# Performance work log

Measured on AMD Instinct MI355X. Metric: run time of the kernel, lower is better.

The kernel has to match this reference:

```python
import jax, jax.numpy as jnp
import numpy as np

DIM = 384
HEADS = 12
WIN = (2, 7, 7)
MLP_RATIO = 4.0
EPS = 1e-5


def _rel_index(Wt, Wh, Ww):
    t, h, w = np.meshgrid(np.arange(Wt), np.arange(Wh), np.arange(Ww), indexing='ij')
    coords = np.stack([t, h, w]).reshape(3, -1).T  # (N,3)
    rel = coords[:, None] - coords[None]  # (N,N,3)
    rel[..., 0] += Wt - 1
    rel[..., 1] += Wh - 1
    rel[..., 2] += Ww - 1
    rel[..., 0] *= (2 * Wh - 1) * (2 * Ww - 1)
    rel[..., 1] *= (2 * Ww - 1)
    return rel.sum(-1)  # (N,N) int


def setup_inputs() -> dict:
    key = jax.random.key(0)
    ks = jax.random.split(key, 16)
    d = DIM
    hdim = int(d * MLP_RATIO)
    Wt, Wh, Ww = WIN
    table_size = (2 * Wt - 1) * (2 * Wh - 1) * (2 * Ww - 1)
    s = lambda fan: 1.0 / np.sqrt(fan)
    return {
        'x': jax.random.normal(ks[0], (2, 8, 56, 56, d), jnp.float32),
        'norm1_g': jnp.ones((d,), jnp.float32),
        'norm1_b': jnp.zeros((d,), jnp.float32),
        'qkv_w': jax.random.normal(ks[1], (d, 3 * d), jnp.float32) * s(d),
        'qkv_b': jnp.zeros((3 * d,), jnp.float32),
        'proj_w': jax.random.normal(ks[2], (d, d), jnp.float32) * s(d),
        'proj_b': jnp.zeros((d,), jnp.float32),
        'bias_table': jax.random.normal(ks[3], (table_size, HEADS), jnp.float32) * 0.02,
        'norm2_g': jnp.ones((d,), jnp.float32),
        'norm2_b': jnp.zeros((d,), jnp.float32),
        'fc1_w': jax.random.normal(ks[4], (d, hdim), jnp.float32) * s(d),
        'fc1_b': jnp.zeros((hdim,), jnp.float32),
        'fc2_w': jax.random.normal(ks[5], (hdim, d), jnp.float32) * s(hdim),
        'fc2_b': jnp.zeros((d,), jnp.float32),
        'rel_index': jnp.asarray(_rel_index(*WIN), jnp.int32),
    }


def _ln(x, g, b):
    mu = x.mean(-1, keepdims=True)
    var = ((x - mu) ** 2).mean(-1, keepdims=True)
    return (x - mu) * jax.lax.rsqrt(var + EPS) * g + b


def _window_partition(x, win):
    B, T, H, W, C = x.shape
    Wt, Wh, Ww = win
    x = x.reshape(B, T // Wt, Wt, H // Wh, Wh, W // Ww, Ww, C)
    x = x.transpose(0, 1, 3, 5, 2, 4, 6, 7)
    return x.reshape(-1, Wt * Wh * Ww, C)


def _window_reverse(win_x, win, B, T, H, W):
    Wt, Wh, Ww = win
    C = win_x.shape[-1]
    x = win_x.reshape(B, T // Wt, H // Wh, W // Ww, Wt, Wh, Ww, C)
    x = x.transpose(0, 1, 4, 2, 5, 3, 6, 7)
    return x.reshape(B, T, H, W, C)


def reference(x, norm1_g, norm1_b, qkv_w, qkv_b, proj_w, proj_b, bias_table,
              norm2_g, norm2_b, fc1_w, fc1_b, fc2_w, fc2_b, rel_index):
    B, T, H, W, C = x.shape
    Wt, Wh, Ww = WIN
    N = Wt * Wh * Ww
    shift = (Wt // 2, Wh // 2, Ww // 2)
    head_dim = C // HEADS
    scale = head_dim ** -0.5

    shortcut = x
    h = _ln(x, norm1_g, norm1_b)
    h = jnp.roll(h, shift=(-shift[0], -shift[1], -shift[2]), axis=(1, 2, 3))
    # dims chosen divisible by window -> no padding branch
    wins = _window_partition(h, WIN)  # (BnW, N, C)
    BnW = wins.shape[0]

    qkv = wins @ qkv_w + qkv_b  # (BnW, N, 3C)
    qkv = qkv.reshape(BnW, N, 3, HEADS, head_dim).transpose(2, 0, 3, 1, 4)
    q, k, v = qkv[0] * scale, qkv[1], qkv[2]  # (BnW, H, N, d)

    bias = bias_table[rel_index.reshape(-1)].reshape(N, N, HEADS).transpose(2, 0, 1)
    attn = jnp.einsum('bhnd,bhmd->bhnm', q, k) + bias[None]
    attn = jax.nn.softmax(attn, axis=-1)
    out = jnp.einsum('bhnm,bhmd->bhnd', attn, v)
    out = out.transpose(0, 2, 1, 3).reshape(BnW, N, C)
    out = out @ proj_w + proj_b

    h = _window_reverse(out.reshape(-1, Wt, Wh, Ww, C), WIN, B, T, H, W)
    h = jnp.roll(h, shift=shift, axis=(1, 2, 3))
    x = shortcut + h

    h2 = _ln(x, norm2_g, norm2_b)
    h2 = jax.nn.gelu(h2 @ fc1_w + fc1_b, approximate=False) @ fc2_w + fc2_b
    return x + h2
```

## Files before the change

### kernel.cpp

```cpp
#include <hip/hip_runtime.h>
#include <cstdint>
#include <cstddef>


typedef __bf16 bf16x8 __attribute__((ext_vector_type(8)));
typedef __bf16 bf16x4 __attribute__((ext_vector_type(4)));
typedef float f32x4 __attribute__((ext_vector_type(4)));

#define DIM 384
#define QKV_DIM 1152
#define HID 1536
#define NHEADS 12
#define NTOK 50176
#define NWIN 512

__device__ __forceinline__ void gload16(const void* g, void* s) {
  __builtin_amdgcn_global_load_lds(
      (const __attribute__((address_space(1))) void*)g,
      (__attribute__((address_space(3))) void*)s, 16, 0, 0);
}

__global__ __launch_bounds__(256) void build_tokmap_k(int* __restrict__ map) {
  int t = blockIdx.x * 256 + threadIdx.x;
  if (t >= NTOK) return;
  int win = t / 98, n = t - win * 98;
  int b = win >> 8, tw = (win >> 6) & 3, hw = (win >> 3) & 7, ww = win & 7;
  int dt = n / 49; int rem = n - dt * 49; int dh = rem / 7, dw = rem - dh * 7;
  int t0 = (tw * 2 + dt + 1) & 7;
  int h0 = hw * 7 + dh + 3; if (h0 >= 56) h0 -= 56;
  int w0 = ww * 7 + dw + 3; if (w0 >= 56) w0 -= 56;
  map[t] = ((b * 8 + t0) * 56 + h0) * 56 + w0;
}

__global__ __launch_bounds__(256) void expand_biasp_k(const float* __restrict__ table,
                                                      const int* __restrict__ rel,
                                                      float* __restrict__ out) {
  int e = blockIdx.x * 256 + threadIdx.x;
  if (e >= NHEADS * 49 * 256) return;
  int r = e & 3, l = (e >> 2) & 63;
  int rest = e >> 8;
  int ni = rest % 7, mi = (rest / 7) % 7, h = rest / 49;
  int i = mi * 16 + (l >> 4) * 4 + r;
  int j = ni * 16 + (l & 15);
  float v;
  if (j >= 98) v = -1e30f;
  else if (i >= 98) v = 0.f;
  else v = table[rel[i * 98 + j] * NHEADS + h];
  out[e] = v;
}

__global__ __launch_bounds__(256) void pack_w64_k(const float* __restrict__ W,
                                                  __bf16* __restrict__ WP,
                                                  int K, int N, int nk,
                                                  int scaleCols, float scale) {
  int idx = blockIdx.x * 256 + threadIdx.x;
  if (idx >= (K * N) >> 3) return;
  int l = idx & 63, f = (idx >> 6) & 7;
  int rest = idx >> 9, kt = rest % nk, cn = rest / nk;
  int n = f >> 1, kk = f & 1;
  int col = cn * 64 + n * 16 + (l & 15);
  int k0 = kt * 64 + (kk * 4 + (l >> 4)) * 8;
  float sc = (col < scaleCols) ? scale : 1.0f;
  bf16x8 v;
  #pragma unroll
  for (int j = 0; j < 8; ++j)
    v[j] = (__bf16)(W[(size_t)(k0 + j) * N + col] * sc);
  *(bf16x8*)(WP + (size_t)idx * 8) = v;
}

__global__ __launch_bounds__(256) void scale_bias_k(const float* __restrict__ b,
                                                    float* __restrict__ out,
                                                    int n, int scaleCols, float scale) {
  int e = blockIdx.x * 256 + threadIdx.x;
  if (e >= n) return;
  out[e] = b[e] * (e < scaleCols ? scale : 1.0f);
}

__global__ __launch_bounds__(384) void vtrans_k(const __bf16* __restrict__ qkv,
                                                __bf16* __restrict__ vt) {
  __shared__ __align__(1024) char T[98304];
  int win = blockIdx.x, t = threadIdx.x;
  const __bf16* base = qkv + (size_t)win * 98 * QKV_DIM + 768 + t;
  #pragma unroll
  for (int c = 0; c < 16; ++c) {
    bf16x8 pk;
    #pragma unroll
    for (int e2 = 0; e2 < 8; ++e2) {
      int tok = c * 8 + e2;
      pk[e2] = (tok < 98) ? base[(size_t)tok * QKV_DIM] : (__bf16)0.f;
    }
    *(bf16x8*)(T + t * 256 + ((c ^ (t & 15)) << 4)) = pk;
  }
  __syncthreads();
  char* wb = (char*)(vt + (size_t)win * 49152);
  #pragma unroll
  for (int i = 0; i < 16; ++i) {
    int g = i * 6144 + t * 16;
    int row = g >> 8, p = (g >> 4) & 15;
    bf16x8 v = *(const bf16x8*)(T + row * 256 + (p << 4));
    int lc = p ^ (row & 15);
    *(bf16x8*)(wb + row * 256 + (lc << 4)) = v;
  }
}

template <typename T, bool MAP>
__global__ __launch_bounds__(256) void ln_pack_k(const T* __restrict__ x,
                                                 const float* __restrict__ g,
                                                 const float* __restrict__ bta,
                                                 __bf16* __restrict__ outp,
                                                 const int* __restrict__ map) {
  const int w = threadIdx.x >> 6, l = threadIdx.x & 63;
  const int tok = blockIdx.x * 32 + w * 8 + (l >> 3);
  const int src = MAP ? map[tok] : tok;
  const T* row = x + (size_t)src * DIM;
  const int o0 = l & 7;
  float v[6][8];
  float s = 0.f;
  #pragma unroll
  for (int j = 0; j < 6; ++j) {
    const int c = (o0 + 8 * j) * 8;
    if constexpr (sizeof(T) == 4) {
      f32x4 p0 = *(const f32x4*)(row + c);
      f32x4 p1 = *(const f32x4*)(row + c + 4);
      #pragma unroll
      for (int e = 0; e < 4; ++e) { v[j][e] = p0[e]; v[j][e + 4] = p1[e]; }
    } else {
      bf16x8 p = *(const bf16x8*)(row + c);
      #pragma unroll
      for (int e = 0; e < 8; ++e) v[j][e] = (float)p[e];
    }
    #pragma unroll
    for (int e = 0; e < 8; ++e) s += v[j][e];
  }
  s += __shfl_xor(s, 1, 64); s += __shfl_xor(s, 2, 64); s += __shfl_xor(s, 4, 64);
  const float mu = s * (1.f / DIM);
  float var = 0.f;
  #pragma unroll
  for (int j = 0; j < 6; ++j)
    #pragma unroll
    for (int e = 0; e < 8; ++e) { float d = v[j][e] - mu; var += d * d; }
  var += __shfl_xor(var, 1, 64); var += __shfl_xor(var, 2, 64); var += __shfl_xor(var, 4, 64);
  const float rs = rsqrtf(var * (1.f / DIM) + 1e-5f);
  const int mg = tok >> 6, m = (tok >> 4) & 3, lr = tok & 15;
  const int kk = o0 >> 2, lg = o0 & 3;
  __bf16* dst = outp + (size_t)mg * 24576 + (m * 2 + kk) * 512 + (lg * 16 + lr) * 8;
  #pragma unroll
  for (int j = 0; j < 6; ++j) {
    const int c = (o0 + 8 * j) * 8;
    f32x4 g0 = *(const f32x4*)(g + c), g1 = *(const f32x4*)(g + c + 4);
    f32x4 b0 = *(const f32x4*)(bta + c), b1 = *(const f32x4*)(bta + c + 4);
    bf16x8 ov;
    #pragma unroll
    for (int e = 0; e < 4; ++e) {
      ov[e] = (__bf16)((v[j][e] - mu) * rs * g0[e] + b0[e]);
      ov[e + 4] = (__bf16)((v[j][e + 4] - mu) * rs * g1[e] + b1[e]);
    }
    *(bf16x8*)(dst + (size_t)j * 4096) = ov;
  }
}

template <int EPI>
__global__ __launch_bounds__(256) void gemm_stream_k(const __bf16* __restrict__ AP,
                                                     const __bf16* __restrict__ WP,
                                                     const float* __restrict__ bias,
                                                     int N,
                                                     __bf16* __restrict__ outb) {
  __shared__ __align__(1024) char lds[32768];
  const int tid = threadIdx.x;
  const int l = tid & 63, w = tid >> 6;
  const int lr = l & 15, lg = l >> 4;
  const int ntile = N >> 6;
  const int nwg = gridDim.x, qd = nwg >> 3, rm = nwg & 7;
  const int xcd = blockIdx.x & 7;
  const int wgid = (xcd < rm ? xcd * (qd + 1) : rm * (qd + 1) + (xcd - rm) * qd)
                   + (blockIdx.x >> 3);
  const int bm = wgid / ntile, bn = wgid - bm * ntile;
  const int mg = bm * 4 + w;
  const int m0 = mg << 6, n0 = bn << 6;
  const __bf16* pA = AP + (size_t)mg * 24576 + l * 8;
  const __bf16* pB = WP + (size_t)bn * 24576 + l * 8;

  bf16x8 a[2][8], b[2][8];
  f32x4 acc[4][4] = {};
  #pragma unroll
  for (int f = 0; f < 8; ++f) {
    a[0][f] = *(const bf16x8*)(pA + f * 512);
    b[0][f] = *(const bf16x8*)(pB + f * 512);
  }
  #pragma unroll
  for (int kt = 0; kt < 6; ++kt) {
    const int cur = kt & 1, nxt = cur ^ 1;
    if (kt < 5) {
      const size_t ko = (size_t)(kt + 1) * 4096;
      #pragma unroll
      for (int f = 0; f < 8; ++f) {
        a[nxt][f] = *(const bf16x8*)(pA + ko + f * 512);
        b[nxt][f] = *(const bf16x8*)(pB + ko + f * 512);
      }
      asm volatile("s_waitcnt vmcnt(16)" ::: "memory");
    } else {
      asm volatile("s_waitcnt vmcnt(0)" ::: "memory");
    }
    __builtin_amdgcn_sched_barrier(0);
    __builtin_amdgcn_s_setprio(1);
    #pragma unroll
    for (int kk = 0; kk < 2; ++kk)
      #pragma unroll
      for (int m = 0; m < 4; ++m)
        #pragma unroll
        for (int n = 0; n < 4; ++n)
          acc[m][n] = __builtin_amdgcn_mfma_f32_16x16x32_bf16(
              b[cur][n * 2 + kk], a[cur][m * 2 + kk], acc[m][n], 0, 0, 0);
    __builtin_amdgcn_s_setprio(0);
  }

  char* abuf = lds + (w << 13);
  #pragma unroll
  for (int m = 0; m < 4; ++m) {
    const int row = (m << 4) + lr;
    #pragma unroll
    for (int n = 0; n < 4; ++n) {
      const int gcol = n0 + (n << 4) + (lg << 2);
      f32x4 a4 = acc[m][n] + *(const f32x4*)(bias + gcol);
      bf16x4 c;
      if (EPI == 2) {
        #pragma unroll
        for (int r = 0; r < 4; ++r) {
          float vv = a4[r];
          float y = vv * (1.0f + 0.044715f * vv * vv);
          c[r] = (__bf16)(vv / (1.0f + __expf(-1.5957691216057308f * y)));
        }
      } else {
        #pragma unroll
        for (int r = 0; r < 4; ++r) c[r] = (__bf16)a4[r];
      }
      const int ch = (n << 1) + (lg >> 1);
      *(bf16x4*)(abuf + (row << 7) + ((ch ^ (row & 7)) << 4) + ((lg & 1) << 3)) = c;
    }
  }
  asm volatile("s_waitcnt lgkmcnt(0)" ::: "memory");
  __builtin_amdgcn_sched_barrier(0);
  #pragma unroll
  for (int i = 0; i < 8; ++i) {
    const int row = (i << 3) + (l >> 3);
    const int p = (l & 7) ^ (row & 7);
    bf16x8 v = *(const bf16x8*)(abuf + (row << 7) + (p << 4));
    *(bf16x8*)(outb + (size_t)(m0 + row) * N + n0 + ((l & 7) << 3)) = v;
  }
}

template <int EPI>
__global__ __launch_bounds__(256) void gemm_k(const __bf16* __restrict__ A,
                                              const __bf16* __restrict__ WP,
                                              const float* __restrict__ bias,
                                              int M, int N, int K,
                                              __bf16* __restrict__ outb,
                                              float* __restrict__ outf,
                                              const float* __restrict__ residf,
                                              const __bf16* __restrict__ residb,
                                              const int* __restrict__ tokmap) {
  __shared__ __align__(1024) char lds[32768];
  const int tid = threadIdx.x;
  const int l = tid & 63, w = tid >> 6;
  const int lr = l & 15, lg = l >> 4;
  const int ntile = N >> 6;
  const int nwg = gridDim.x, qd = nwg >> 3, rm = nwg & 7;
  const int xcd = blockIdx.x & 7;
  const int wgid = (xcd < rm ? xcd * (qd + 1) : rm * (qd + 1) + (xcd - rm) * qd)
                   + (blockIdx.x >> 3);
  const int bm = wgid / ntile, bn = wgid - bm * ntile;
  const int m0 = (bm << 8) + (w << 6);
  const int n0 = bn << 6;
  const int nk = K >> 6;
  const int sch = (l & 7) ^ ((l >> 3) & 7);
  const __bf16* pa = A + (size_t)(m0 + (l >> 3)) * K + sch * 8;
  char* abuf = lds + (w << 13);
  const __bf16* pB = WP + (size_t)bn * nk * 4096 + l * 8;

#define STAGEA(kt)                                                   \
  { const size_t ko_ = (size_t)(kt) << 6;                            \
    _Pragma("unroll")                                                \
    for (int s_ = 0; s_ < 8; ++s_)                                   \
      gload16(pa + (size_t)(s_ * 8) * K + ko_, abuf + s_ * 1024); }
#define LOADB(kt)                                                    \
  { const __bf16* p_ = pB + (size_t)(kt) * 4096;                     \
    _Pragma("unroll")                                                \
    for (int f_ = 0; f_ < 8; ++f_)                                   \
      b[f_] = *(const bf16x8*)(p_ + f_ * 512); }
#define LDA()                                                        \
  { _Pragma("unroll")                                                \
    for (int kk_ = 0; kk_ < 2; ++kk_) {                              \
      const int ck_ = (kk_ << 2) + lg;                               \
      _Pragma("unroll")                                              \
      for (int m_ = 0; m_ < 4; ++m_) {                               \
        int r_ = (m_ << 4) + lr;                                     \
        a[m_][kk_] = *(const bf16x8*)(abuf + (r_ << 7) +             \
                                      ((ck_ ^ (r_ & 7)) << 4));      \
      } }                                                            \
    asm volatile("s_waitcnt lgkmcnt(0)" ::: "memory");               \
    __builtin_amdgcn_sched_barrier(0); }

  bf16x8 a[4][2], b[8];
  f32x4 acc[4][4] = {};
  STAGEA(0)
  asm volatile("s_waitcnt vmcnt(0)" ::: "memory");
  LDA()
  for (int kt = 0; kt < nk; ++kt) {
    LOADB(kt)
    const bool pf = (kt + 1 < nk);
    if (pf) STAGEA(kt + 1)
    __builtin_amdgcn_s_setprio(1);
    #pragma unroll
    for (int kk = 0; kk < 2; ++kk)
      #pragma unroll
      for (int m = 0; m < 4; ++m)
        #pragma unroll
        for (int n = 0; n < 4; ++n)
          acc[m][n] = __builtin_amdgcn_mfma_f32_16x16x32_bf16(b[n * 2 + kk], a[m][kk],
                                                              acc[m][n], 0, 0, 0);
    __builtin_amdgcn_s_setprio(0);
    if (pf) {
      asm volatile("s_waitcnt vmcnt(0)" ::: "memory");
      LDA()
    }
  }
#undef STAGEA
#undef LOADB
#undef LDA

  if (EPI == 3) {
    #pragma unroll
    for (int hh = 0; hh < 2; ++hh) {
      #pragma unroll
      for (int m = 0; m < 4; ++m) {
        const int row = (m << 4) + lr;
        #pragma unroll
        for (int n2 = 0; n2 < 2; ++n2) {
          const int n = (hh << 1) + n2;
          const int gcol = n0 + (n << 4) + (lg << 2);
          f32x4 a4 = acc[m][n] + *(const f32x4*)(bias + gcol);
          const int ch = (n2 << 2) + lg;
          *(f32x4*)(abuf + (row << 7) + ((ch ^ (row & 7)) << 4)) = a4;
        }
      }
      asm volatile("s_waitcnt lgkmcnt(0)" ::: "memory");
      __builtin_amdgcn_sched_barrier(0);
      #pragma unroll
      for (int i = 0; i < 8; ++i) {
        const int row = (i << 3) + (l >> 3);
        const int p = (l & 7) ^ (row & 7);
        f32x4 v = *(const f32x4*)(abuf + (row << 7) + (p << 4));
        const int grow = m0 + row;
        const int gcol = n0 + (hh << 5) + ((l & 7) << 2);
        bf16x4 sv = *(const bf16x4*)(residb + (size_t)grow * N + gcol);
        f32x4 o;
        #pragma unroll
        for (int r = 0; r < 4; ++r) o[r] = v[r] + (float)sv[r];
        *(f32x4*)(outf + (size_t)grow * N + gcol) = o;
      }
      if (hh == 0) {
        asm volatile("s_waitcnt lgkmcnt(0)" ::: "memory");
        __builtin_amdgcn_sched_barrier(0);
      }
    }
  } else {
    #pragma unroll
    for (int m = 0; m < 4; ++m) {
      const int row = (m << 4) + lr;
      #pragma unroll
      for (int n = 0; n < 4; ++n) {
        const int gcol = n0 + (n << 4) + (lg << 2);
        f32x4 a4 = acc[m][n] + *(const f32x4*)(bias + gcol);
        bf16x4 c;
        #pragma unroll
        for (int r = 0; r < 4; ++r) c[r] = (__bf16)a4[r];
        const int ch = (n << 1) + (lg >> 1);
        *(bf16x4*)(abuf + (row << 7) + ((ch ^ (row & 7)) << 4) + ((lg & 1) << 3)) = c;
      }
    }
    asm volatile("s_waitcnt lgkmcnt(0)" ::: "memory");
    __builtin_amdgcn_sched_barrier(0);
    #pragma unroll
    for (int i = 0; i < 8; ++i) {
      const int row = (i << 3) + (l >> 3);
      const int p = (l & 7) ^ (row & 7);
      bf16x8 v = *(const bf16x8*)(abuf + (row << 7) + (p << 4));
      const int gcol = n0 + ((l & 7) << 3);
      const int dst = tokmap[m0 + row];
      const float* rp = residf + (size_t)dst * N + gcol;
      f32x4 r0 = *(const f32x4*)rp, r1 = *(const f32x4*)(rp + 4);
      bf16x8 c2;
      #pragma unroll
      for (int j = 0; j < 4; ++j) {
        c2[j] = (__bf16)(r0[j] + (float)v[j]);
        c2[j + 4] = (__bf16)(r1[j] + (float)v[j + 4]);
      }
      *(bf16x8*)(outb + (size_t)dst * N + gcol) = c2;
    }
  }
}

__global__ __launch_bounds__(64) void attn_k(const __bf16* __restrict__ qkv,
                                             const __bf16* __restrict__ vt,
                                             const float* __restrict__ pb,
                                             __bf16* __restrict__ out) {
  __shared__ __align__(1024) char P[4096];
  const int l = threadIdx.x, lr = l & 15, lg = l >> 4;
  const int bid = blockIdx.x;
  const int xc = bid & 7, kk = bid >> 3;
  const int wh = (kk / 7) * 8 + xc, mi = kk % 7;
  const int win = wh / NHEADS, h = wh - win * NHEADS;
  const size_t wbase = (size_t)win * 98 * QKV_DIM;
  const __bf16* qb = qkv + wbase + h * 32;
  const __bf16* kb = qb + 384;
  const bf16x8 z8 = {};
  const f32x4 fz = {};

  bf16x8 kf[7];
  #pragma unroll
  for (int ni = 0; ni < 7; ++ni) {
    int tok = ni * 16 + lr;
    kf[ni] = (tok < 98) ? *(const bf16x8*)(kb + (size_t)tok * QKV_DIM + lg * 8) : z8;
  }
  int qt = mi * 16 + lr;
  bf16x8 qf = (qt < 98) ? *(const bf16x8*)(qb + (size_t)qt * QKV_DIM + lg * 8) : z8;
  const f32x4* pbp = (const f32x4*)pb + (size_t)((h * 7 + mi) * 7) * 64 + l;
  f32x4 bv[7];
  #pragma unroll
  for (int ni = 0; ni < 7; ++ni) bv[ni] = pbp[ni * 64];

  f32x4 s[7];
  #pragma unroll
  for (int ni = 0; ni < 7; ++ni)
    s[ni] = __builtin_amdgcn_mfma_f32_16x16x32_bf16(qf, kf[ni], fz, 0, 0, 0);

  if (l < 32) {
    int row = l >> 1, c = 14 + (l & 1);
    *(f32x4*)(P + row * 256 + ((c ^ (row & 7)) << 4)) = fz;
  }

  #pragma unroll
  for (int r = 0; r < 4; ++r) {
    float mx = -1e30f;
    #pragma unroll
    for (int ni = 0; ni < 7; ++ni) {
      float vv = s[ni][r] + bv[ni][r];
      s[ni][r] = vv;
      mx = fmaxf(mx, vv);
    }
    #pragma unroll
    for (int m2 = 1; m2 < 16; m2 <<= 1) mx = fmaxf(mx, __shfl_xor(mx, m2, 64));
    float sum = 0.f;
    #pragma unroll
    for (int ni = 0; ni < 7; ++ni) { float p = __expf(s[ni][r] - mx); s[ni][r] = p; sum += p; }
    #pragma unroll
    for (int m2 = 1; m2 < 16; m2 <<= 1) sum += __shfl_xor(sum, m2, 64);
    float inv = 1.0f / sum;
    int il = lg * 4 + r;
    #pragma unroll
    for (int ni = 0; ni < 7; ++ni) {
      int j = ni * 16 + lr;
      *(__bf16*)(P + il * 256 + (((j >> 3) ^ (il & 7)) << 4) + ((j & 7) << 1)) =
          (__bf16)(s[ni][r] * inv);
    }
  }
  __syncthreads();

  bf16x8 pa[4];
  #pragma unroll
  for (int ks = 0; ks < 4; ++ks) {
    int ck = ks * 4 + lg;
    pa[ks] = *(const bf16x8*)(P + lr * 256 + ((ck ^ (lr & 7)) << 4));
  }
  const __bf16* vrow = vt + ((size_t)wh * 32) * 128;
  f32x4 oo[2];
  #pragma unroll
  for (int nf = 0; nf < 2; ++nf) {
    int d = nf * 16 + lr;
    f32x4 o = fz;
    #pragma unroll
    for (int ks = 0; ks < 4; ++ks) {
      bf16x8 vb = *(const bf16x8*)(vrow + (size_t)d * 128 + ks * 32 + lg * 8);
      o = __builtin_amdgcn_mfma_f32_16x16x32_bf16(pa[ks], vb, o, 0, 0, 0);
    }
    oo[nf] = o;
  }
  #pragma unroll
  for (int nf = 0; nf < 2; ++nf)
    #pragma unroll
    for (int r = 0; r < 4; ++r)
      *(__bf16*)(P + (lg * 4 + r) * 64 + (((nf << 4) + lr) << 1)) = (__bf16)oo[nf][r];
  asm volatile("s_waitcnt lgkmcnt(0)" ::: "memory");
  __builtin_amdgcn_sched_barrier(0);
  {
    const int row = l >> 2;
    bf16x8 v = *(const bf16x8*)(P + row * 64 + ((l & 3) << 4));
    const int tok = mi * 16 + row;
    if (tok < 98)
      *(bf16x8*)(out + ((size_t)win * 98 + tok) * DIM + h * 32 + ((l & 3) << 3)) = v;
  }
}

extern "C" void kernel_launch(void* const* d_in, const int* in_sizes, int n_in,
                              void* d_out, int out_size, void* d_ws, size_t ws_size,
                              hipStream_t stream) {
  const float* x      = (const float*)d_in[0];
  const float* n1g    = (const float*)d_in[1];
  const float* n1b    = (const float*)d_in[2];
  const float* qkv_w  = (const float*)d_in[3];
  const float* qkv_b  = (const float*)d_in[4];
  const float* proj_w = (const float*)d_in[5];
  const float* proj_b = (const float*)d_in[6];
  const float* btab   = (const float*)d_in[7];
  const float* n2g    = (const float*)d_in[8];
  const float* n2b    = (const float*)d_in[9];
  const float* fc1_w  = (const float*)d_in[10];
  const float* fc1_b  = (const float*)d_in[11];
  const float* fc2_w  = (const float*)d_in[12];
  const float* fc2_b  = (const float*)d_in[13];
  const int*   relidx = (const int*)d_in[14];
  float* outp = (float*)d_out;
  (void)in_sizes; (void)n_in; (void)out_size; (void)ws_size;

  char* ws = (char*)d_ws;
  size_t off = 0;
  auto alloc = [&](size_t bytes) {
    char* p = ws + off;
    off = (off + bytes + 255) & ~(size_t)255;
    return p;
  };
  int*    tokmap  = (int*)alloc((size_t)NTOK * 4);
  float*  biasex  = (float*)alloc((size_t)NHEADS * 49 * 256 * 4);
  __bf16* wqkvP   = (__bf16*)alloc((size_t)QKV_DIM * DIM * 2);
  __bf16* wprojP  = (__bf16*)alloc((size_t)DIM * DIM * 2);
  __bf16* wfc1P   = (__bf16*)alloc((size_t)HID * DIM * 2);
  __bf16* wfc2P   = (__bf16*)alloc((size_t)DIM * HID * 2);
  float*  qkvbS   = (float*)alloc((size_t)QKV_DIM * 4);
  __bf16* tokens  = (__bf16*)alloc((size_t)NTOK * DIM * 2);
  __bf16* qkvbuf  = (__bf16*)alloc((size_t)NTOK * HID * 2);
  __bf16* s1      = (__bf16*)alloc((size_t)NTOK * DIM * 2);
  __bf16* tokens2 = (__bf16*)alloc((size_t)NTOK * DIM * 2);
  __bf16* attnout = tokens;
  __bf16* h1 = qkvbuf;
  __bf16* vt = (__bf16*)d_out;

  const float scale = 0.17677669529663687f;

  build_tokmap_k<<<NTOK / 256, 256, 0, stream>>>(tokmap);
  expand_biasp_k<<<(NHEADS * 49 * 256) / 256, 256, 0, stream>>>(btab, relidx, biasex);
  pack_w64_k<<<(DIM * QKV_DIM / 8) / 256, 256, 0, stream>>>(qkv_w, wqkvP, DIM, QKV_DIM, 6, DIM, scale);
  pack_w64_k<<<(DIM * DIM / 8) / 256, 256, 0, stream>>>(proj_w, wprojP, DIM, DIM, 6, 0, 1.0f);
  pack_w64_k<<<(DIM * HID / 8) / 256, 256, 0, stream>>>(fc1_w, wfc1P, DIM, HID, 6, 0, 1.0f);
  pack_w64_k<<<(HID * DIM / 8) / 256, 256, 0, stream>>>(fc2_w, wfc2P, HID, DIM, 24, 0, 1.0f);
  scale_bias_k<<<(QKV_DIM + 255) / 256, 256, 0, stream>>>(qkv_b, qkvbS, QKV_DIM, DIM, scale);

  ln_pack_k<float, true><<<NTOK / 32, 256, 0, stream>>>(x, n1g, n1b, tokens, tokmap);
  gemm_stream_k<0><<<(NTOK / 256) * (QKV_DIM / 64), 256, 0, stream>>>(
      tokens, wqkvP, qkvbS, QKV_DIM, qkvbuf);
  vtrans_k<<<NWIN, 384, 0, stream>>>(qkvbuf, vt);
  attn_k<<<NWIN * NHEADS * 7, 64, 0, stream>>>(qkvbuf, vt, biasex, attnout);
  gemm_k<1><<<(NTOK / 256) * (DIM / 64), 256, 0, stream>>>(
      attnout, wprojP, proj_b, NTOK, DIM, DIM, s1, nullptr, x, nullptr, tokmap);
  ln_pack_k<__bf16, false><<<NTOK / 32, 256, 0, stream>>>(s1, n2g, n2b, tokens2, nullptr);
  gemm_stream_k<2><<<(NTOK / 256) * (HID / 64), 256, 0, stream>>>(
      tokens2, wfc1P, fc1_b, HID, h1);
  gemm_k<3><<<(NTOK / 256) * (DIM / 64), 256, 0, stream>>>(
      h1, wfc2P, fc2_b, NTOK, DIM, HID, nullptr, outp, nullptr, s1, nullptr);
}
```

Baseline: 472.6 us.

## Write fc1 output pre-packed and run fc2 through streaming GEMM kernel

The fc1 GEMM epilogue now writes its GELU output directly in the MFMA-fragment packed layout. This lets the fc2 GEMM use the register-streaming kernel (templated on K-tile count, NK=24) instead of the LDS-staged gemm_k path. The goal is to remove the LDS staging and swizzle work on the A operand for the largest-K GEMM. In exchange, fc1 stores become tile-packed rather than row-major, and fc2 keeps two 8-fragment register buffers per operand across 24 K steps, which raises register pressure.

```diff
diff --git a/kernel.cpp b/kernel.cpp
--- a/kernel.cpp
+++ b/kernel.cpp
@@ -159,12 +159,14 @@
   }
 }
 
-template <int EPI>
+template <int EPI, int NK>
 __global__ __launch_bounds__(256) void gemm_stream_k(const __bf16* __restrict__ AP,
                                                      const __bf16* __restrict__ WP,
                                                      const float* __restrict__ bias,
                                                      int N,
-                                                     __bf16* __restrict__ outb) {
+                                                     __bf16* __restrict__ outb,
+                                                     float* __restrict__ outf,
+                                                     const __bf16* __restrict__ residb) {
   __shared__ __align__(1024) char lds[32768];
   const int tid = threadIdx.x;
   const int l = tid & 63, w = tid >> 6;
@@ -177,8 +179,8 @@
   const int bm = wgid / ntile, bn = wgid - bm * ntile;
   const int mg = bm * 4 + w;
   const int m0 = mg << 6, n0 = bn << 6;
-  const __bf16* pA = AP + (size_t)mg * 24576 + l * 8;
-  const __bf16* pB = WP + (size_t)bn * 24576 + l * 8;
+  const __bf16* pA = AP + (size_t)mg * (NK * 4096) + l * 8;
+  const __bf16* pB = WP + (size_t)bn * (NK * 4096) + l * 8;
 
   bf16x8 a[2][8], b[2][8];
   f32x4 acc[4][4] = {};
@@ -188,9 +190,9 @@
     b[0][f] = *(const bf16x8*)(pB + f * 512);
   }
   #pragma unroll
-  for (int kt = 0; kt < 6; ++kt) {
+  for (int kt = 0; kt < NK; ++kt) {
     const int cur = kt & 1, nxt = cur ^ 1;
-    if (kt < 5) {
+    if (kt < NK - 1) {
       const size_t ko = (size_t)(kt + 1) * 4096;
       #pragma unroll
       for (int f = 0; f < 8; ++f) {
@@ -215,50 +217,95 @@
   }
 
   char* abuf = lds + (w << 13);
-  #pragma unroll
-  for (int m = 0; m < 4; ++m) {
-    const int row = (m << 4) + lr;
-    #pragma unroll
-    for (int n = 0; n < 4; ++n) {
-      const int gcol = n0 + (n << 4) + (lg << 2);
-      f32x4 a4 = acc[m][n] + *(const f32x4*)(bias + gcol);
-      bf16x4 c;
-      if (EPI == 2) {
+  if (EPI == 3) {
+    #pragma unroll
+    for (int hh = 0; hh < 2; ++hh) {
+      #pragma unroll
+      for (int m = 0; m < 4; ++m) {
+        const int row = (m << 4) + lr;
         #pragma unroll
-        for (int r = 0; r < 4; ++r) {
-          float vv = a4[r];
-          float y = vv * (1.0f + 0.044715f * vv * vv);
-          c[r] = (__bf16)(vv / (1.0f + __expf(-1.5957691216057308f * y)));
+        for (int n2 = 0; n2 < 2; ++n2) {
+          const int n = (hh << 1) + n2;
+          const int gcol = n0 + (n << 4) + (lg << 2);
+          f32x4 a4 = acc[m][n] + *(const f32x4*)(bias + gcol);
+          const int ch = (n2 << 2) + lg;
+          *(f32x4*)(abuf + (row << 7) + ((ch ^ (row & 7)) << 4)) = a4;
         }
-      } else {
+      }
+      asm volatile("s_waitcnt lgkmcnt(0)" ::: "memory");
+      __builtin_amdgcn_sched_barrier(0);
+      #pragma unroll
+      for (int i = 0; i < 8; ++i) {
+        const int row = (i << 3) + (l >> 3);
+        const int p = (l & 7) ^ (row & 7);
+        f32x4 v = *(const f32x4*)(abuf + (row << 7) + (p << 4));
+        const int grow = m0 + row;
+        const int gcol = n0 + (hh << 5) + ((l & 7) << 2);
+        bf16x4 sv = *(const bf16x4*)(residb + (size_t)grow * N + gcol);
+        f32x4 o;
         #pragma unroll
-        for (int r = 0; r < 4; ++r) c[r] = (__bf16)a4[r];
-      }
-      const int ch = (n << 1) + (lg >> 1);
-      *(bf16x4*)(abuf + (row << 7) + ((ch ^ (row & 7)) << 4) + ((lg & 1) << 3)) = c;
-    }
-  }
-  asm volatile("s_waitcnt lgkmcnt(0)" ::: "memory");
-  __builtin_amdgcn_sched_barrier(0);
-  #pragma unroll
-  for (int i = 0; i < 8; ++i) {
-    const int row = (i << 3) + (l >> 3);
-    const int p = (l & 7) ^ (row & 7);
-    bf16x8 v = *(const bf16x8*)(abuf + (row << 7) + (p << 4));
-    *(bf16x8*)(outb + (size_t)(m0 + row) * N + n0 + ((l & 7) << 3)) = v;
-  }
-}
-
-template <int EPI>
-__global__ __launch_bounds__(256) void gemm_k(const __bf16* __restrict__ A,
-                                              const __bf16* __restrict__ WP,
-                                              const float* __restrict__ bias,
-                                              int M, int N, int K,
-                                              __bf16* __restrict__ outb,
-                                              float* __restrict__ outf,
-                                              const float* __restrict__ residf,
-                                              const __bf16* __restrict__ residb,
-                                              const int* __restrict__ tokmap) {
+        for (int r = 0; r < 4; ++r) o[r] = v[r] + (float)sv[r];
+        *(f32x4*)(outf + (size_t)grow * N + gcol) = o;
+      }
+      if (hh == 0) {
+        asm volatile("s_waitcnt lgkmcnt(0)" ::: "memory");
+        __builtin_amdgcn_sched_barrier(0);
+      }
+    }
+  } else {
+    #pragma unroll
+    for (int m = 0; m < 4; ++m) {
+      const int row = (m << 4) + lr;
+      #pragma unroll
+      for (int n = 0; n < 4; ++n) {
+        const int gcol = n0 + (n << 4) + (lg << 2);
+        f32x4 a4 = acc[m][n] + *(const f32x4*)(bias + gcol);
+        bf16x4 c;
+        if (EPI == 4) {
+          #pragma unroll
+          for (int r = 0; r < 4; ++r) {
+            float vv = a4[r];
+            float y = vv * (1.0f + 0.044715f * vv * vv);
+            c[r] = (__bf16)(vv / (1.0f + __expf(-1.5957691216057308f * y)));
+          }
+        } else {
+          #pragma unroll
+          for (int r = 0; r < 4; ++r) c[r] = (__bf16)a4[r];
+        }
+        const int ch = (n << 1) + (lg >> 1);
+        *(bf16x4*)(abuf + (row << 7) + ((ch ^ (row & 7)) << 4) + ((lg & 1) << 3)) = c;
+      }
+    }
+    asm volatile("s_waitcnt lgkmcnt(0)" ::: "memory");
+    __builtin_amdgcn_sched_barrier(0);
+    if (EPI == 4) {
+      #pragma unroll
+      for (int f = 0; f < 8; ++f) {
+        const int row = ((f >> 1) << 4) + lr;
+        const int lc = ((f & 1) << 2) + (l >> 4);
+        const int ph = lc ^ (row & 7);
+        bf16x8 v = *(const bf16x8*)(abuf + (row << 7) + (ph << 4));
+        *(bf16x8*)(outb + ((size_t)(mg * 24 + bn) * 8 + f) * 512 + l * 8) = v;
+      }
+    } else {
+      #pragma unroll
+      for (int i = 0; i < 8; ++i) {
+        const int row = (i << 3) + (l >> 3);
+        const int p = (l & 7) ^ (row & 7);
+        bf16x8 v = *(const bf16x8*)(abuf + (row << 7) + (p << 4));
+        *(bf16x8*)(outb + (size_t)(m0 + row) * N + n0 + ((l & 7) << 3)) = v;
+      }
+    }
+  }
+}
+
+__global__ __launch_bounds__(256) void gemm_proj_k(const __bf16* __restrict__ A,
+                                                   const __bf16* __restrict__ WP,
+                                                   const float* __restrict__ bias,
+                                                   int M, int N, int K,
+                                                   __bf16* __restrict__ outb,
+                                                   const float* __restrict__ residf,
+                                                   const int* __restrict__ tokmap) {
   __shared__ __align__(1024) char lds[32768];
   const int tid = threadIdx.x;
   const int l = tid & 63, w = tid >> 6;
@@ -328,75 +375,38 @@
 #undef LOADB
 #undef LDA
 
-  if (EPI == 3) {
-    #pragma unroll
-    for (int hh = 0; hh < 2; ++hh) {
-      #pragma unroll
-      for (int m = 0; m < 4; ++m) {
-        const int row = (m << 4) + lr;
-        #pragma unroll
-        for (int n2 = 0; n2 < 2; ++n2) {
-          const int n = (hh << 1) + n2;
-          const int gcol = n0 + (n << 4) + (lg << 2);
-          f32x4 a4 = acc[m][n] + *(const f32x4*)(bias + gcol);
-          const int ch = (n2 << 2) + lg;
-          *(f32x4*)(abuf + (row << 7) + ((ch ^ (row & 7)) << 4)) = a4;
-        }
-      }
-      asm volatile("s_waitcnt lgkmcnt(0)" ::: "memory");
-      __builtin_amdgcn_sched_barrier(0);
-      #pragma unroll
-      for (int i = 0; i < 8; ++i) {
-        const int row = (i << 3) + (l >> 3);
-        const int p = (l & 7) ^ (row & 7);
-        f32x4 v = *(const f32x4*)(abuf + (row << 7) + (p << 4));
-        const int grow = m0 + row;
-        const int gcol = n0 + (hh << 5) + ((l & 7) << 2);
-        bf16x4 sv = *(const bf16x4*)(residb + (size_t)grow * N + gcol);
-        f32x4 o;
-        #pragma unroll
-        for (int r = 0; r < 4; ++r) o[r] = v[r] + (float)sv[r];
-        *(f32x4*)(outf + (size_t)grow * N + gcol) = o;
-      }
-      if (hh == 0) {
-        asm volatile("s_waitcnt lgkmcnt(0)" ::: "memory");
-        __builtin_amdgcn_sched_barrier(0);
-      }
-    }
-  } else {
-    #pragma unroll
-    for (int m = 0; m < 4; ++m) {
-      const int row = (m << 4) + lr;
-      #pragma unroll
-      for (int n = 0; n < 4; ++n) {
-        const int gcol = n0 + (n << 4) + (lg << 2);
-        f32x4 a4 = acc[m][n] + *(const f32x4*)(bias + gcol);
-        bf16x4 c;
-        #pragma unroll
-        for (int r = 0; r < 4; ++r) c[r] = (__bf16)a4[r];
-        const int ch = (n << 1) + (lg >> 1);
-        *(bf16x4*)(abuf + (row << 7) + ((ch ^ (row & 7)) << 4) + ((lg & 1) << 3)) = c;
-      }
-    }
-    asm volatile("s_waitcnt lgkmcnt(0)" ::: "memory");
-    __builtin_amdgcn_sched_barrier(0);
-    #pragma unroll
-    for (int i = 0; i < 8; ++i) {
-      const int row = (i << 3) + (l >> 3);
-      const int p = (l & 7) ^ (row & 7);
-      bf16x8 v = *(const bf16x8*)(abuf + (row << 7) + (p << 4));
-      const int gcol = n0 + ((l & 7) << 3);
-      const int dst = tokmap[m0 + row];
-      const float* rp = residf + (size_t)dst * N + gcol;
-      f32x4 r0 = *(const f32x4*)rp, r1 = *(const f32x4*)(rp + 4);
-      bf16x8 c2;
-      #pragma unroll
-      for (int j = 0; j < 4; ++j) {
-        c2[j] = (__bf16)(r0[j] + (float)v[j]);
-        c2[j + 4] = (__bf16)(r1[j] + (float)v[j + 4]);
-      }
-      *(bf16x8*)(outb + (size_t)dst * N + gcol) = c2;
-    }
+  #pragma unroll
+  for (int m = 0; m < 4; ++m) {
+    const int row = (m << 4) + lr;
+    #pragma unroll
+    for (int n = 0; n < 4; ++n) {
+      const int gcol = n0 + (n << 4) + (lg << 2);
+      f32x4 a4 = acc[m][n] + *(const f32x4*)(bias + gcol);
+      bf16x4 c;
+      #pragma unroll
+      for (int r = 0; r < 4; ++r) c[r] = (__bf16)a4[r];
+      const int ch = (n << 1) + (lg >> 1);
+      *(bf16x4*)(abuf + (row << 7) + ((ch ^ (row & 7)) << 4) + ((lg & 1) << 3)) = c;
+    }
+  }
+  asm volatile("s_waitcnt lgkmcnt(0)" ::: "memory");
+  __builtin_amdgcn_sched_barrier(0);
+  #pragma unroll
+  for (int i = 0; i < 8; ++i) {
+    const int row = (i << 3) + (l >> 3);
+    const int p = (l & 7) ^ (row & 7);
+    bf16x8 v = *(const bf16x8*)(abuf + (row << 7) + (p << 4));
+    const int gcol = n0 + ((l & 7) << 3);
+    const int dst = tokmap[m0 + row];
+    const float* rp = residf + (size_t)dst * N + gcol;
+    f32x4 r0 = *(const f32x4*)rp, r1 = *(const f32x4*)(rp + 4);
+    bf16x8 c2;
+    #pragma unroll
+    for (int j = 0; j < 4; ++j) {
+      c2[j] = (__bf16)(r0[j] + (float)v[j]);
+      c2[j + 4] = (__bf16)(r1[j] + (float)v[j + 4]);
+    }
+    *(bf16x8*)(outb + (size_t)dst * N + gcol) = c2;
   }
 }
 
@@ -541,7 +551,7 @@
   __bf16* s1      = (__bf16*)alloc((size_t)NTOK * DIM * 2);
   __bf16* tokens2 = (__bf16*)alloc((size_t)NTOK * DIM * 2);
   __bf16* attnout = tokens;
-  __bf16* h1 = qkvbuf;
+  __bf16* h1P = qkvbuf;
   __bf16* vt = (__bf16*)d_out;
 
   const float scale = 0.17677669529663687f;
@@ -555,15 +565,15 @@
   scale_bias_k<<<(QKV_DIM + 255) / 256, 256, 0, stream>>>(qkv_b, qkvbS, QKV_DIM, DIM, scale);
 
   ln_pack_k<float, true><<<NTOK / 32, 256, 0, stream>>>(x, n1g, n1b, tokens, tokmap);
-  gemm_stream_k<0><<<(NTOK / 256) * (QKV_DIM / 64), 256, 0, stream>>>(
-      tokens, wqkvP, qkvbS, QKV_DIM, qkvbuf);
+  gemm_stream_k<0, 6><<<(NTOK / 256) * (QKV_DIM / 64), 256, 0, stream>>>(
+      tokens, wqkvP, qkvbS, QKV_DIM, qkvbuf, nullptr, nullptr);
   vtrans_k<<<NWIN, 384, 0, stream>>>(qkvbuf, vt);
   attn_k<<<NWIN * NHEADS * 7, 64, 0, stream>>>(qkvbuf, vt, biasex, attnout);
-  gemm_k<1><<<(NTOK / 256) * (DIM / 64), 256, 0, stream>>>(
-      attnout, wprojP, proj_b, NTOK, DIM, DIM, s1, nullptr, x, nullptr, tokmap);
+  gemm_proj_k<<<(NTOK / 256) * (DIM / 64), 256, 0, stream>>>(
+      attnout, wprojP, proj_b, NTOK, DIM, DIM, s1, x, tokmap);
   ln_pack_k<__bf16, false><<<NTOK / 32, 256, 0, stream>>>(s1, n2g, n2b, tokens2, nullptr);
-  gemm_stream_k<2><<<(NTOK / 256) * (HID / 64), 256, 0, stream>>>(
-      tokens2, wfc1P, fc1_b, HID, h1);
-  gemm_k<3><<<(NTOK / 256) * (DIM / 64), 256, 0, stream>>>(
-      h1, wfc2P, fc2_b, NTOK, DIM, HID, nullptr, outp, nullptr, s1, nullptr);
-}
+  gemm_stream_k<4, 6><<<(NTOK / 256) * (HID / 64), 256, 0, stream>>>(
+      tokens2, wfc1P, fc1_b, HID, h1P, nullptr, nullptr);
+  gemm_stream_k<3, 24><<<(NTOK / 256) * (DIM / 64), 256, 0, stream>>>(
+      h1P, wfc2P, fc2_b, DIM, nullptr, outp, s1);
+}
```

Result: faster. 455.2 us (-3.7%).
